# Kernel optimization log

Hardware: AMD Instinct MI355X
Metric: run time of the kernel (lower is better)

Reference implementation:

```python
import jax, jax.numpy as jnp
import numpy as np


def setup_inputs() -> dict:
    key = jax.random.key(0)
    k1, k2, k3 = jax.random.split(key, 3)
    B, M, J = 4096, 64, 24  # batch, n_max_markers, n_joints
    points = jax.random.normal(k1, (B, M, 3), dtype=jnp.float32)
    weight = jax.random.uniform(k2, (B, M, J), dtype=jnp.float32)  # positive soft weights
    offset = jax.random.normal(k3, (B, M, J, 3), dtype=jnp.float32)
    return {"points": points, "weight": weight, "offset": offset}


def reference(points, weight, offset):
    # P: per-joint marker offsets (B, J, 3, M); Q: world marker positions (B, 1, 3, M)
    P = jnp.transpose(offset, (0, 2, 3, 1))
    Q = jnp.transpose(points, (0, 2, 1))[:, None]
    w = jnp.transpose(weight, (0, 2, 1))[:, :, None]  # (B, J, 1, M)

    wsum = jnp.sum(w, axis=-1)                   # (B, J, 1)
    P_ = jnp.sum(P * w, axis=-1) / wsum          # (B, J, 3) weighted centroid of offsets
    Q_ = jnp.sum(Q * w, axis=-1) / wsum          # (B, J, 3) weighted centroid of markers

    X = P - P_[..., None]                        # (B, J, 3, M)
    Y = Q - Q_[..., None]                        # (B, J, 3, M) via broadcast

    # Cross-covariance S = X @ Y^T (NOTE: original multiplies un-weighted centered coords)
    S = jnp.einsum('bjdm,bjem->bjde', X, Y)      # (B, J, 3, 3)

    U, _, Vh = jnp.linalg.svd(S)
    V = jnp.swapaxes(Vh, -1, -2)
    Ut = jnp.swapaxes(U, -1, -2)
    det = jnp.linalg.det(jnp.matmul(V, Ut))      # (B, J) reflection correction
    Ut = Ut.at[..., -1, :].multiply(det[..., None])
    R = jnp.matmul(V, Ut)                        # (B, J, 3, 3) optimal rotation
    t = Q_[..., None] - jnp.matmul(R, P_[..., None])  # (B, J, 3, 1)
    return R, t
```

## Files before the change

kernel.cpp:

```cpp
#include <hip/hip_runtime.h>


constexpr int M = 64;
constexpr int J = 24;
constexpr int KS = 4;
constexpr int SPB = 64;
constexpr int NACC = 22;

template<int P, int Q>
__device__ __forceinline__ void jrot(float A[4][4], float V[4][4]) {
    float apq = A[P][Q];
    float theta = (A[Q][Q] - A[P][P]) / (2.0f * apq);
    float t = 1.0f / (fabsf(theta) + sqrtf(theta * theta + 1.0f));
    t = (theta < 0.0f) ? -t : t;
    t = (apq == 0.0f) ? 0.0f : t;
    float c = 1.0f / sqrtf(t * t + 1.0f);
    float s = t * c;
#pragma unroll
    for (int k = 0; k < 4; ++k) {
        float akp = A[k][P], akq = A[k][Q];
        A[k][P] = c * akp - s * akq;
        A[k][Q] = s * akp + c * akq;
    }
#pragma unroll
    for (int k = 0; k < 4; ++k) {
        float apk = A[P][k], aqk = A[Q][k];
        A[P][k] = c * apk - s * aqk;
        A[Q][k] = s * apk + c * aqk;
        float vkp = V[k][P], vkq = V[k][Q];
        V[k][P] = c * vkp - s * vkq;
        V[k][Q] = s * vkp + c * vkq;
    }
}

__global__ __launch_bounds__(256) void kabsch_kernel(
    const float* __restrict__ points,
    const float* __restrict__ weight,
    const float* __restrict__ offset,
    float* __restrict__ out,
    int bj_total)
{
    __shared__ float lds[NACC][SPB * KS];

    const int t = threadIdx.x;
    const int s = t >> 2;
    const int k = t & 3;
    const int bj = blockIdx.x * SPB + s;

    float acc[NACC];
#pragma unroll
    for (int n = 0; n < NACC; ++n) acc[n] = 0.0f;

    if (bj < bj_total) {
        const int b = bj / J;
        const int j = bj - b * J;
        const float* wq = weight + (size_t)b * M * J + k * J + j;
        const float* oq = offset + ((size_t)b * M * J + k * J + j) * 3;
        const float* pq = points + (size_t)b * M * 3 + k * 3;

#pragma unroll 4
        for (int i = 0; i < M / KS; ++i) {
            float w  = wq[i * (KS * J)];
            float o0 = oq[i * (KS * J * 3) + 0];
            float o1 = oq[i * (KS * J * 3) + 1];
            float o2 = oq[i * (KS * J * 3) + 2];
            float p0 = pq[i * (KS * 3) + 0];
            float p1 = pq[i * (KS * 3) + 1];
            float p2 = pq[i * (KS * 3) + 2];
            acc[0] += w;
            acc[1] = fmaf(w, o0, acc[1]); acc[2] = fmaf(w, o1, acc[2]); acc[3] = fmaf(w, o2, acc[3]);
            acc[4] = fmaf(w, p0, acc[4]); acc[5] = fmaf(w, p1, acc[5]); acc[6] = fmaf(w, p2, acc[6]);
            acc[7] += o0; acc[8] += o1; acc[9] += o2;
            acc[10] += p0; acc[11] += p1; acc[12] += p2;
            acc[13] = fmaf(o0, p0, acc[13]); acc[14] = fmaf(o0, p1, acc[14]); acc[15] = fmaf(o0, p2, acc[15]);
            acc[16] = fmaf(o1, p0, acc[16]); acc[17] = fmaf(o1, p1, acc[17]); acc[18] = fmaf(o1, p2, acc[18]);
            acc[19] = fmaf(o2, p0, acc[19]); acc[20] = fmaf(o2, p1, acc[20]); acc[21] = fmaf(o2, p2, acc[21]);
        }
    }

#pragma unroll
    for (int n = 0; n < NACC; ++n) lds[n][t] = acc[n];

    __syncthreads();

    if (t >= SPB) return;

    const int bj0 = blockIdx.x * SPB + t;
    if (bj0 >= bj_total) return;
    const int b0 = bj0 / J;
    const int j0 = bj0 - b0 * J;
    (void)j0;

    float T[NACC];
#pragma unroll
    for (int n = 0; n < NACC; ++n) {
        float4 v = *reinterpret_cast<const float4*>(&lds[n][t * 4]);
        T[n] = (v.x + v.y) + (v.z + v.w);
    }

    const float W = T[0];
    const float inv = 1.0f / W;
    const float cP0 = T[1] * inv, cP1 = T[2] * inv, cP2 = T[3] * inv;
    const float cQ0 = T[4] * inv, cQ1 = T[5] * inv, cQ2 = T[6] * inv;
    const float To0 = T[7], To1 = T[8], To2 = T[9];
    const float Tp0 = T[10], Tp1 = T[11], Tp2 = T[12];

    const float fM = (float)M;
    float S00 = T[13] - cP0 * Tp0 - cQ0 * To0 + fM * cP0 * cQ0;
    float S01 = T[14] - cP0 * Tp1 - cQ1 * To0 + fM * cP0 * cQ1;
    float S02 = T[15] - cP0 * Tp2 - cQ2 * To0 + fM * cP0 * cQ2;
    float S10 = T[16] - cP1 * Tp0 - cQ0 * To1 + fM * cP1 * cQ0;
    float S11 = T[17] - cP1 * Tp1 - cQ1 * To1 + fM * cP1 * cQ1;
    float S12 = T[18] - cP1 * Tp2 - cQ2 * To1 + fM * cP1 * cQ2;
    float S20 = T[19] - cP2 * Tp0 - cQ0 * To2 + fM * cP2 * cQ0;
    float S21 = T[20] - cP2 * Tp1 - cQ1 * To2 + fM * cP2 * cQ1;
    float S22 = T[21] - cP2 * Tp2 - cQ2 * To2 + fM * cP2 * cQ2;

    float A[4][4], V[4][4];
    A[0][0] = S00 + S11 + S22;
    A[0][1] = A[1][0] = S12 - S21;
    A[0][2] = A[2][0] = S20 - S02;
    A[0][3] = A[3][0] = S01 - S10;
    A[1][1] = S00 - S11 - S22;
    A[1][2] = A[2][1] = S01 + S10;
    A[1][3] = A[3][1] = S02 + S20;
    A[2][2] = -S00 + S11 - S22;
    A[2][3] = A[3][2] = S12 + S21;
    A[3][3] = -S00 - S11 + S22;

#pragma unroll
    for (int r = 0; r < 4; ++r)
#pragma unroll
        for (int c = 0; c < 4; ++c)
            V[r][c] = (r == c) ? 1.0f : 0.0f;

#pragma unroll 1
    for (int sweep = 0; sweep < 8; ++sweep) {
        jrot<0, 1>(A, V); jrot<0, 2>(A, V); jrot<0, 3>(A, V);
        jrot<1, 2>(A, V); jrot<1, 3>(A, V); jrot<2, 3>(A, V);
    }

    float best = A[0][0];
    float qw = V[0][0], qx = V[1][0], qy = V[2][0], qz = V[3][0];
#pragma unroll
    for (int i = 1; i < 4; ++i) {
        bool better = A[i][i] > best;
        best = better ? A[i][i] : best;
        qw = better ? V[0][i] : qw;
        qx = better ? V[1][i] : qx;
        qy = better ? V[2][i] : qy;
        qz = better ? V[3][i] : qz;
    }
    float nrm = 1.0f / sqrtf(qw * qw + qx * qx + qy * qy + qz * qz);
    qw *= nrm; qx *= nrm; qy *= nrm; qz *= nrm;

    float R00 = 1.f - 2.f * (qy * qy + qz * qz);
    float R01 = 2.f * (qx * qy - qw * qz);
    float R02 = 2.f * (qx * qz + qw * qy);
    float R10 = 2.f * (qx * qy + qw * qz);
    float R11 = 1.f - 2.f * (qx * qx + qz * qz);
    float R12 = 2.f * (qy * qz - qw * qx);
    float R20 = 2.f * (qx * qz - qw * qy);
    float R21 = 2.f * (qy * qz + qw * qx);
    float R22 = 1.f - 2.f * (qx * qx + qy * qy);

    float* Rout = out + (size_t)bj0 * 9;
    Rout[0] = R00; Rout[1] = R01; Rout[2] = R02;
    Rout[3] = R10; Rout[4] = R11; Rout[5] = R12;
    Rout[6] = R20; Rout[7] = R21; Rout[8] = R22;

    float t0 = cQ0 - (R00 * cP0 + R01 * cP1 + R02 * cP2);
    float t1 = cQ1 - (R10 * cP0 + R11 * cP1 + R12 * cP2);
    float t2 = cQ2 - (R20 * cP0 + R21 * cP1 + R22 * cP2);
    float* tout = out + (size_t)bj_total * 9 + (size_t)bj0 * 3;
    tout[0] = t0; tout[1] = t1; tout[2] = t2;
}

extern "C" void kernel_launch(void* const* d_in, const int* in_sizes, int n_in,
                              void* d_out, int out_size, void* d_ws, size_t ws_size,
                              hipStream_t stream) {
    const float* points = (const float*)d_in[0];
    const float* weight = (const float*)d_in[1];
    const float* offset = (const float*)d_in[2];
    float* out = (float*)d_out;

    int B = in_sizes[0] / (M * 3);
    int bj_total = B * J;
    int block = SPB * KS;
    int grid = (bj_total + SPB - 1) / SPB;
    kabsch_kernel<<<grid, block, 0, stream>>>(points, weight, offset, out, bj_total);
}
```

Measured before the change: 154.7 us.

## Split into LDS-staged accumulation kernel and separate per-pair eigen-solve kernel

Accumulation now runs one block per batch element. The block stages weight, offset and points into padded shared memory with coalesced float4 loads, reduces 22 moments over 8 marker slices, and writes the 3x3 covariance and centroids to workspace. A second small kernel runs the Horn quaternion Jacobi solve, one thread per (batch, joint), so that divergent work no longer idles a 256-thread block. Jacobi sweeps drop from 8 to 6 and the divisions and square roots use fast rcp/rsq intrinsics, which may reduce accuracy. There is a fused one-thread-per-pair fallback when the workspace is too small. The split adds a second launch and a workspace round trip.

```diff
diff --git a/kernel.cpp b/kernel.cpp
--- a/kernel.cpp
+++ b/kernel.cpp
@@ -3,18 +3,136 @@
 
 constexpr int M = 64;
 constexpr int J = 24;
-constexpr int KS = 4;
-constexpr int SPB = 64;
 constexpr int NACC = 22;
+constexpr int NWS  = 15;
+
+constexpr int WSTR = 27;
+constexpr int OSTR = 73;
+constexpr int WLEN = M * WSTR;
+constexpr int OLEN = M * OSTR;
+constexpr int PLEN = M * 3;
+constexpr int KSP  = 8;
+constexpr int RED  = KSP * J;
+
+__global__ __launch_bounds__(256) void accum_kernel(
+    const float* __restrict__ points,
+    const float* __restrict__ weight,
+    const float* __restrict__ offset,
+    float* __restrict__ ws,
+    int bj_total)
+{
+    __shared__ float smem[WLEN + OLEN + PLEN];
+    float* lw = smem;
+    float* lo = smem + WLEN;
+    float* lp = smem + WLEN + OLEN;
+    float* red = smem + WLEN;
+
+    const int t = threadIdx.x;
+    const int b = blockIdx.x;
+
+    const float4* wg = (const float4*)(weight + (size_t)b * (M * J));
+    for (int idx = t; idx < (M * J) / 4; idx += 256) {
+        float4 v = wg[idx];
+        int g0 = idx * 4;
+#pragma unroll
+        for (int c = 0; c < 4; ++c) {
+            int g = g0 + c;
+            int m = g / J, r = g - m * J;
+            lw[m * WSTR + r] = (&v.x)[c];
+        }
+    }
+    const float4* og = (const float4*)(offset + (size_t)b * (M * J * 3));
+    for (int idx = t; idx < (M * J * 3) / 4; idx += 256) {
+        float4 v = og[idx];
+        int g0 = idx * 4;
+#pragma unroll
+        for (int c = 0; c < 4; ++c) {
+            int g = g0 + c;
+            int m = g / (J * 3), r = g - m * (J * 3);
+            lo[m * OSTR + r] = (&v.x)[c];
+        }
+    }
+    const float4* pg = (const float4*)(points + (size_t)b * (M * 3));
+    if (t < PLEN / 4) ((float4*)lp)[t] = pg[t];
+
+    __syncthreads();
+
+    float acc[NACC];
+#pragma unroll
+    for (int n = 0; n < NACC; ++n) acc[n] = 0.0f;
+
+    if (t < KSP * J) {
+        const int j = t % J;
+        const int k = t / J;
+#pragma unroll
+        for (int i = 0; i < M / KSP; ++i) {
+            const int m = k * (M / KSP) + i;
+            float w  = lw[m * WSTR + j];
+            float o0 = lo[m * OSTR + j * 3 + 0];
+            float o1 = lo[m * OSTR + j * 3 + 1];
+            float o2 = lo[m * OSTR + j * 3 + 2];
+            float p0 = lp[m * 3 + 0];
+            float p1 = lp[m * 3 + 1];
+            float p2 = lp[m * 3 + 2];
+            acc[0] += w;
+            acc[1] = fmaf(w, o0, acc[1]);  acc[2] = fmaf(w, o1, acc[2]);  acc[3] = fmaf(w, o2, acc[3]);
+            acc[4] = fmaf(w, p0, acc[4]);  acc[5] = fmaf(w, p1, acc[5]);  acc[6] = fmaf(w, p2, acc[6]);
+            acc[7] += o0; acc[8] += o1; acc[9] += o2;
+            acc[10] += p0; acc[11] += p1; acc[12] += p2;
+            acc[13] = fmaf(o0, p0, acc[13]); acc[14] = fmaf(o0, p1, acc[14]); acc[15] = fmaf(o0, p2, acc[15]);
+            acc[16] = fmaf(o1, p0, acc[16]); acc[17] = fmaf(o1, p1, acc[17]); acc[18] = fmaf(o1, p2, acc[18]);
+            acc[19] = fmaf(o2, p0, acc[19]); acc[20] = fmaf(o2, p1, acc[20]); acc[21] = fmaf(o2, p2, acc[21]);
+        }
+    }
+
+    __syncthreads();
+    if (t < KSP * J) {
+#pragma unroll
+        for (int n = 0; n < NACC; ++n) red[n * RED + t] = acc[n];
+    }
+    __syncthreads();
+
+    if (t < J) {
+        float T[NACC];
+#pragma unroll
+        for (int n = 0; n < NACC; ++n) {
+            float s = 0.0f;
+#pragma unroll
+            for (int k = 0; k < KSP; ++k) s += red[n * RED + k * J + t];
+            T[n] = s;
+        }
+        const float inv = __builtin_amdgcn_rcpf(T[0]);
+        const float cP0 = T[1] * inv, cP1 = T[2] * inv, cP2 = T[3] * inv;
+        const float cQ0 = T[4] * inv, cQ1 = T[5] * inv, cQ2 = T[6] * inv;
+        const float To0 = T[7], To1 = T[8], To2 = T[9];
+        const float Tp0 = T[10], Tp1 = T[11], Tp2 = T[12];
+        const float fM = (float)M;
+        float Sv[NWS];
+        Sv[0] = T[13] - cP0 * Tp0 - cQ0 * To0 + fM * cP0 * cQ0;
+        Sv[1] = T[14] - cP0 * Tp1 - cQ1 * To0 + fM * cP0 * cQ1;
+        Sv[2] = T[15] - cP0 * Tp2 - cQ2 * To0 + fM * cP0 * cQ2;
+        Sv[3] = T[16] - cP1 * Tp0 - cQ0 * To1 + fM * cP1 * cQ0;
+        Sv[4] = T[17] - cP1 * Tp1 - cQ1 * To1 + fM * cP1 * cQ1;
+        Sv[5] = T[18] - cP1 * Tp2 - cQ2 * To1 + fM * cP1 * cQ2;
+        Sv[6] = T[19] - cP2 * Tp0 - cQ0 * To2 + fM * cP2 * cQ0;
+        Sv[7] = T[20] - cP2 * Tp1 - cQ1 * To2 + fM * cP2 * cQ1;
+        Sv[8] = T[21] - cP2 * Tp2 - cQ2 * To2 + fM * cP2 * cQ2;
+        Sv[9] = cP0;  Sv[10] = cP1; Sv[11] = cP2;
+        Sv[12] = cQ0; Sv[13] = cQ1; Sv[14] = cQ2;
+        const int bj = b * J + t;
+#pragma unroll
+        for (int n = 0; n < NWS; ++n) ws[(size_t)n * bj_total + bj] = Sv[n];
+    }
+}
 
 template<int P, int Q>
 __device__ __forceinline__ void jrot(float A[4][4], float V[4][4]) {
     float apq = A[P][Q];
-    float theta = (A[Q][Q] - A[P][P]) / (2.0f * apq);
-    float t = 1.0f / (fabsf(theta) + sqrtf(theta * theta + 1.0f));
+    float theta = (A[Q][Q] - A[P][P]) * __builtin_amdgcn_rcpf(2.0f * apq);
+    float t = __builtin_amdgcn_rcpf(fabsf(theta) + __builtin_amdgcn_sqrtf(fmaf(theta, theta, 1.0f)));
     t = (theta < 0.0f) ? -t : t;
     t = (apq == 0.0f) ? 0.0f : t;
-    float c = 1.0f / sqrtf(t * t + 1.0f);
+    float c = __builtin_amdgcn_rsqf(fmaf(t, t, 1.0f));
     float s = t * c;
 #pragma unroll
     for (int k = 0; k < 4; ++k) {
@@ -33,89 +151,12 @@
     }
 }
 
-__global__ __launch_bounds__(256) void kabsch_kernel(
-    const float* __restrict__ points,
-    const float* __restrict__ weight,
-    const float* __restrict__ offset,
-    float* __restrict__ out,
-    int bj_total)
+__device__ __forceinline__ void horn_solve(
+    float S00, float S01, float S02, float S10, float S11, float S12,
+    float S20, float S21, float S22,
+    float cP0, float cP1, float cP2, float cQ0, float cQ1, float cQ2,
+    float* __restrict__ Rout, float* __restrict__ tout)
 {
-    __shared__ float lds[NACC][SPB * KS];
-
-    const int t = threadIdx.x;
-    const int s = t >> 2;
-    const int k = t & 3;
-    const int bj = blockIdx.x * SPB + s;
-
-    float acc[NACC];
-#pragma unroll
-    for (int n = 0; n < NACC; ++n) acc[n] = 0.0f;
-
-    if (bj < bj_total) {
-        const int b = bj / J;
-        const int j = bj - b * J;
-        const float* wq = weight + (size_t)b * M * J + k * J + j;
-        const float* oq = offset + ((size_t)b * M * J + k * J + j) * 3;
-        const float* pq = points + (size_t)b * M * 3 + k * 3;
-
-#pragma unroll 4
-        for (int i = 0; i < M / KS; ++i) {
-            float w  = wq[i * (KS * J)];
-            float o0 = oq[i * (KS * J * 3) + 0];
-            float o1 = oq[i * (KS * J * 3) + 1];
-            float o2 = oq[i * (KS * J * 3) + 2];
-            float p0 = pq[i * (KS * 3) + 0];
-            float p1 = pq[i * (KS * 3) + 1];
-            float p2 = pq[i * (KS * 3) + 2];
-            acc[0] += w;
-            acc[1] = fmaf(w, o0, acc[1]); acc[2] = fmaf(w, o1, acc[2]); acc[3] = fmaf(w, o2, acc[3]);
-            acc[4] = fmaf(w, p0, acc[4]); acc[5] = fmaf(w, p1, acc[5]); acc[6] = fmaf(w, p2, acc[6]);
-            acc[7] += o0; acc[8] += o1; acc[9] += o2;
-            acc[10] += p0; acc[11] += p1; acc[12] += p2;
-            acc[13] = fmaf(o0, p0, acc[13]); acc[14] = fmaf(o0, p1, acc[14]); acc[15] = fmaf(o0, p2, acc[15]);
-            acc[16] = fmaf(o1, p0, acc[16]); acc[17] = fmaf(o1, p1, acc[17]); acc[18] = fmaf(o1, p2, acc[18]);
-            acc[19] = fmaf(o2, p0, acc[19]); acc[20] = fmaf(o2, p1, acc[20]); acc[21] = fmaf(o2, p2, acc[21]);
-        }
-    }
-
-#pragma unroll
-    for (int n = 0; n < NACC; ++n) lds[n][t] = acc[n];
-
-    __syncthreads();
-
-    if (t >= SPB) return;
-
-    const int bj0 = blockIdx.x * SPB + t;
-    if (bj0 >= bj_total) return;
-    const int b0 = bj0 / J;
-    const int j0 = bj0 - b0 * J;
-    (void)j0;
-
-    float T[NACC];
-#pragma unroll
-    for (int n = 0; n < NACC; ++n) {
-        float4 v = *reinterpret_cast<const float4*>(&lds[n][t * 4]);
-        T[n] = (v.x + v.y) + (v.z + v.w);
-    }
-
-    const float W = T[0];
-    const float inv = 1.0f / W;
-    const float cP0 = T[1] * inv, cP1 = T[2] * inv, cP2 = T[3] * inv;
-    const float cQ0 = T[4] * inv, cQ1 = T[5] * inv, cQ2 = T[6] * inv;
-    const float To0 = T[7], To1 = T[8], To2 = T[9];
-    const float Tp0 = T[10], Tp1 = T[11], Tp2 = T[12];
-
-    const float fM = (float)M;
-    float S00 = T[13] - cP0 * Tp0 - cQ0 * To0 + fM * cP0 * cQ0;
-    float S01 = T[14] - cP0 * Tp1 - cQ1 * To0 + fM * cP0 * cQ1;
-    float S02 = T[15] - cP0 * Tp2 - cQ2 * To0 + fM * cP0 * cQ2;
-    float S10 = T[16] - cP1 * Tp0 - cQ0 * To1 + fM * cP1 * cQ0;
-    float S11 = T[17] - cP1 * Tp1 - cQ1 * To1 + fM * cP1 * cQ1;
-    float S12 = T[18] - cP1 * Tp2 - cQ2 * To1 + fM * cP1 * cQ2;
-    float S20 = T[19] - cP2 * Tp0 - cQ0 * To2 + fM * cP2 * cQ0;
-    float S21 = T[20] - cP2 * Tp1 - cQ1 * To2 + fM * cP2 * cQ1;
-    float S22 = T[21] - cP2 * Tp2 - cQ2 * To2 + fM * cP2 * cQ2;
-
     float A[4][4], V[4][4];
     A[0][0] = S00 + S11 + S22;
     A[0][1] = A[1][0] = S12 - S21;
@@ -127,7 +168,6 @@
     A[2][2] = -S00 + S11 - S22;
     A[2][3] = A[3][2] = S12 + S21;
     A[3][3] = -S00 - S11 + S22;
-
 #pragma unroll
     for (int r = 0; r < 4; ++r)
 #pragma unroll
@@ -135,7 +175,7 @@
             V[r][c] = (r == c) ? 1.0f : 0.0f;
 
 #pragma unroll 1
-    for (int sweep = 0; sweep < 8; ++sweep) {
+    for (int sweep = 0; sweep < 6; ++sweep) {
         jrot<0, 1>(A, V); jrot<0, 2>(A, V); jrot<0, 3>(A, V);
         jrot<1, 2>(A, V); jrot<1, 3>(A, V); jrot<2, 3>(A, V);
     }
@@ -151,7 +191,7 @@
         qy = better ? V[2][i] : qy;
         qz = better ? V[3][i] : qz;
     }
-    float nrm = 1.0f / sqrtf(qw * qw + qx * qx + qy * qy + qz * qz);
+    float nrm = __builtin_amdgcn_rsqf(qw * qw + qx * qx + qy * qy + qz * qz);
     qw *= nrm; qx *= nrm; qy *= nrm; qz *= nrm;
 
     float R00 = 1.f - 2.f * (qy * qy + qz * qz);
@@ -164,16 +204,80 @@
     float R21 = 2.f * (qy * qz + qw * qx);
     float R22 = 1.f - 2.f * (qx * qx + qy * qy);
 
-    float* Rout = out + (size_t)bj0 * 9;
     Rout[0] = R00; Rout[1] = R01; Rout[2] = R02;
     Rout[3] = R10; Rout[4] = R11; Rout[5] = R12;
     Rout[6] = R20; Rout[7] = R21; Rout[8] = R22;
-
-    float t0 = cQ0 - (R00 * cP0 + R01 * cP1 + R02 * cP2);
-    float t1 = cQ1 - (R10 * cP0 + R11 * cP1 + R12 * cP2);
-    float t2 = cQ2 - (R20 * cP0 + R21 * cP1 + R22 * cP2);
-    float* tout = out + (size_t)bj_total * 9 + (size_t)bj0 * 3;
-    tout[0] = t0; tout[1] = t1; tout[2] = t2;
+    tout[0] = cQ0 - (R00 * cP0 + R01 * cP1 + R02 * cP2);
+    tout[1] = cQ1 - (R10 * cP0 + R11 * cP1 + R12 * cP2);
+    tout[2] = cQ2 - (R20 * cP0 + R21 * cP1 + R22 * cP2);
+}
+
+__global__ __launch_bounds__(64) void solve_kernel(
+    const float* __restrict__ ws, float* __restrict__ out, int bj_total)
+{
+    int tid = blockIdx.x * 64 + threadIdx.x;
+    if (tid >= bj_total) return;
+    float Sv[NWS];
+#pragma unroll
+    for (int n = 0; n < NWS; ++n) Sv[n] = ws[(size_t)n * bj_total + tid];
+    float Rr[9], tr[3];
+    horn_solve(Sv[0], Sv[1], Sv[2], Sv[3], Sv[4], Sv[5], Sv[6], Sv[7], Sv[8],
+               Sv[9], Sv[10], Sv[11], Sv[12], Sv[13], Sv[14], Rr, tr);
+    float* Rout = out + (size_t)tid * 9;
+#pragma unroll
+    for (int n = 0; n < 9; ++n) Rout[n] = Rr[n];
+    float* tout = out + (size_t)bj_total * 9 + (size_t)tid * 3;
+    tout[0] = tr[0]; tout[1] = tr[1]; tout[2] = tr[2];
+}
+
+__global__ __launch_bounds__(256) void fused_kernel(
+    const float* __restrict__ points, const float* __restrict__ weight,
+    const float* __restrict__ offset, float* __restrict__ out, int bj_total)
+{
+    int tid = blockIdx.x * blockDim.x + threadIdx.x;
+    if (tid >= bj_total) return;
+    int b = tid / J, j = tid - b * J;
+    const float* wq = weight + (size_t)b * M * J + j;
+    const float* oq = offset + ((size_t)b * M * J + j) * 3;
+    const float* pq = points + (size_t)b * M * 3;
+    float a[NACC];
+#pragma unroll
+    for (int n = 0; n < NACC; ++n) a[n] = 0.0f;
+#pragma unroll 4
+    for (int m = 0; m < M; ++m) {
+        float w = wq[m * J];
+        float o0 = oq[m * (J * 3) + 0], o1 = oq[m * (J * 3) + 1], o2 = oq[m * (J * 3) + 2];
+        float p0 = pq[m * 3 + 0], p1 = pq[m * 3 + 1], p2 = pq[m * 3 + 2];
+        a[0] += w;
+        a[1] = fmaf(w, o0, a[1]); a[2] = fmaf(w, o1, a[2]); a[3] = fmaf(w, o2, a[3]);
+        a[4] = fmaf(w, p0, a[4]); a[5] = fmaf(w, p1, a[5]); a[6] = fmaf(w, p2, a[6]);
+        a[7] += o0; a[8] += o1; a[9] += o2;
+        a[10] += p0; a[11] += p1; a[12] += p2;
+        a[13] = fmaf(o0, p0, a[13]); a[14] = fmaf(o0, p1, a[14]); a[15] = fmaf(o0, p2, a[15]);
+        a[16] = fmaf(o1, p0, a[16]); a[17] = fmaf(o1, p1, a[17]); a[18] = fmaf(o1, p2, a[18]);
+        a[19] = fmaf(o2, p0, a[19]); a[20] = fmaf(o2, p1, a[20]); a[21] = fmaf(o2, p2, a[21]);
+    }
+    float inv = __builtin_amdgcn_rcpf(a[0]);
+    float cP0 = a[1] * inv, cP1 = a[2] * inv, cP2 = a[3] * inv;
+    float cQ0 = a[4] * inv, cQ1 = a[5] * inv, cQ2 = a[6] * inv;
+    const float fM = (float)M;
+    float S00 = a[13] - cP0 * a[10] - cQ0 * a[7] + fM * cP0 * cQ0;
+    float S01 = a[14] - cP0 * a[11] - cQ1 * a[7] + fM * cP0 * cQ1;
+    float S02 = a[15] - cP0 * a[12] - cQ2 * a[7] + fM * cP0 * cQ2;
+    float S10 = a[16] - cP1 * a[10] - cQ0 * a[8] + fM * cP1 * cQ0;
+    float S11 = a[17] - cP1 * a[11] - cQ1 * a[8] + fM * cP1 * cQ1;
+    float S12 = a[18] - cP1 * a[12] - cQ2 * a[8] + fM * cP1 * cQ2;
+    float S20 = a[19] - cP2 * a[10] - cQ0 * a[9] + fM * cP2 * cQ0;
+    float S21 = a[20] - cP2 * a[11] - cQ1 * a[9] + fM * cP2 * cQ1;
+    float S22 = a[21] - cP2 * a[12] - cQ2 * a[9] + fM * cP2 * cQ2;
+    float Rr[9], tr[3];
+    horn_solve(S00, S01, S02, S10, S11, S12, S20, S21, S22,
+               cP0, cP1, cP2, cQ0, cQ1, cQ2, Rr, tr);
+    float* Rout = out + (size_t)tid * 9;
+#pragma unroll
+    for (int n = 0; n < 9; ++n) Rout[n] = Rr[n];
+    float* tout = out + (size_t)bj_total * 9 + (size_t)tid * 3;
+    tout[0] = tr[0]; tout[1] = tr[1]; tout[2] = tr[2];
 }
 
 extern "C" void kernel_launch(void* const* d_in, const int* in_sizes, int n_in,
@@ -186,7 +290,12 @@
 
     int B = in_sizes[0] / (M * 3);
     int bj_total = B * J;
-    int block = SPB * KS;
-    int grid = (bj_total + SPB - 1) / SPB;
-    kabsch_kernel<<<grid, block, 0, stream>>>(points, weight, offset, out, bj_total);
-}
+
+    size_t need = (size_t)NWS * bj_total * sizeof(float);
+    if (ws_size >= need) {
+        accum_kernel<<<B, 256, 0, stream>>>(points, weight, offset, (float*)d_ws, bj_total);
+        solve_kernel<<<(bj_total + 63) / 64, 64, 0, stream>>>((const float*)d_ws, out, bj_total);
+    } else {
+        fused_kernel<<<(bj_total + 255) / 256, 256, 0, stream>>>(points, weight, offset, out, bj_total);
+    }
+}
```

Measured after the change: 153.7 us. No clear change (-0.6%).
